# Optimization experiments

Hardware: AMD Instinct MI355X
Metric: run time of the kernel (lower is better)

The kernel has to match this reference:

```python
import jax, jax.numpy as jnp
import numpy as np

C_IN = 256   # c_m
C_H = 32     # outer_product_dim
C_Z = 128
B, S, N = 1, 128, 256  # batch, msa depth, n_res
EPS = 1e-5


def setup_inputs() -> dict:
    key = jax.random.key(0)
    ks = jax.random.split(key, 10)
    msa = jax.random.normal(ks[0], (B, S, N, C_IN), dtype=jnp.float32)
    mask = jax.random.uniform(ks[1], (B, S, N), dtype=jnp.float32)
    ln_w = jnp.ones((C_IN,), jnp.float32)
    ln_b = jnp.zeros((C_IN,), jnp.float32)
    # weights stored [in, out] (torch Linear transposed)
    wl = jax.random.normal(ks[2], (C_IN, C_H), jnp.float32) / np.sqrt(C_IN)
    bl = jnp.zeros((C_H,), jnp.float32)
    wr = jax.random.normal(ks[3], (C_IN, C_H), jnp.float32) / np.sqrt(C_IN)
    br = jnp.zeros((C_H,), jnp.float32)
    wo = jax.random.normal(ks[4], (C_H * C_H, C_Z), jnp.float32) / np.sqrt(C_H * C_H)
    bo = jnp.zeros((C_Z,), jnp.float32)
    return {"msa_representation": msa, "msa_mask": mask, "ln_w": ln_w, "ln_b": ln_b,
            "wl": wl, "bl": bl, "wr": wr, "br": br, "wo": wo, "bo": bo}


def _layer_norm(x, w, b):
    mu = jnp.mean(x, axis=-1, keepdims=True)
    var = jnp.var(x, axis=-1, keepdims=True)
    return (x - mu) * jax.lax.rsqrt(var + EPS) * w + b


def reference(msa_representation, msa_mask, ln_w, ln_b, wl, bl, wr, br, wo, bo):
    x = _layer_norm(msa_representation, ln_w, ln_b)            # [b,s,i,c_in]
    A = x @ wl + bl                                            # [b,s,i,c]
    Bm = x @ wr + br                                           # [b,s,j,d]
    m = msa_mask
    A = A * m[..., None]
    Bm = Bm * m[..., None]
    outer = jnp.einsum('bsic,bsjd->bijcd', A, Bm)              # [b,i,j,c,d]
    norm = jnp.clip(jnp.einsum('bsi,bsj->bij', m, m), 1.0, None)
    mean_val = outer / norm[..., None, None]
    b_, i_, j_ = mean_val.shape[:3]
    mean_val = mean_val.reshape(b_, i_, j_, -1)                # [b,i,j,c*d]
    return mean_val @ wo + bo                                  # [b,i,j,c_z]
```

## Files before the change

kernel.cpp:

```cpp
#include <hip/hip_runtime.h>
#include <hip/hip_bf16.h>
#include <stdint.h>

#define SDEP 128
#define NRES 256
#define CZQ 128

typedef __bf16 v8bf __attribute__((ext_vector_type(8)));
typedef __bf16 v4bf __attribute__((ext_vector_type(4)));
typedef float v16f __attribute__((ext_vector_type(16)));

__device__ __forceinline__ float dpp_wave_sum(float x) {
  float t;
#define STEP(ctrl)                                                         \
  t = __builtin_bit_cast(float, __builtin_amdgcn_update_dpp(               \
          0, __builtin_bit_cast(int, x), ctrl, 0xF, 0xF, true));           \
  x += t;
  STEP(0x111)
  STEP(0x112)
  STEP(0x114)
  STEP(0x118)
  STEP(0x142)
  STEP(0x143)
#undef STEP
  return x;
}
__device__ __forceinline__ float lane63(float x) {
  return __builtin_bit_cast(float,
      __builtin_amdgcn_readlane(__builtin_bit_cast(int, x), 63));
}

#define MFMA32(a, b, c) __builtin_amdgcn_mfma_f32_32x32x16_bf16(a, b, c, 0, 0, 0)

__global__ __launch_bounds__(512, 2) void fusedA_kernel(
    const float* __restrict__ msa, const float* __restrict__ lnw,
    const float* __restrict__ lnb, const float* __restrict__ wl,
    const float* __restrict__ wr, const float* __restrict__ mask,
    const float* __restrict__ wo, const float* __restrict__ bl,
    const float* __restrict__ br,
    __bf16* __restrict__ At2, __bf16* __restrict__ Bt2,
    float* __restrict__ rnorm, __bf16* __restrict__ wot4)
{
  __shared__ __bf16 xs[128 * 258];
  __shared__ __bf16 wcs[16384];
  __shared__ __bf16 Ls[8 * 32 * 36];

  const int i = blockIdx.x, t = threadIdx.x;
  const int w = t >> 6, lane = t & 63;
  const int half = lane >> 5, l31 = lane & 31;
  const int sb = w >> 1, nh = w & 1;

  #pragma unroll
  for (int u = 0; u < 32; ++u) {
    int idx = u * 512 + t;
    int j = idx & 7, n = (idx >> 3) & 31, hf = (idx >> 8) & 1;
    int ks = (idx >> 9) & 15, tile = idx >> 13;
    const float* wsrc = tile ? wr : wl;
    wcs[idx] = (__bf16)wsrc[(ks * 16 + hf * 8 + j) * 32 + n];
  }

  const float4 wv4 = ((const float4*)lnw)[lane];
  const float4 bv4 = ((const float4*)lnb)[lane];

  #pragma unroll 8
  for (int r = 0; r < 16; ++r) {
    const int s = sb * 32 + nh * 16 + r;
    float4 x = ((const float4*)(msa + ((size_t)s * 256 + i) * 256))[lane];
    float s1 = dpp_wave_sum(x.x + x.y + x.z + x.w);
    float s2 = dpp_wave_sum(x.x * x.x + x.y * x.y + x.z * x.z + x.w * x.w);
    float mu = lane63(s1) * (1.f / 256.f);
    float var = lane63(s2) * (1.f / 256.f) - mu * mu;
    float rs = rsqrtf(var + 1e-5f);
    v4bf o;
    o[0] = (__bf16)((x.x - mu) * rs * wv4.x + bv4.x);
    o[1] = (__bf16)((x.y - mu) * rs * wv4.y + bv4.y);
    o[2] = (__bf16)((x.z - mu) * rs * wv4.z + bv4.z);
    o[3] = (__bf16)((x.w - mu) * rs * wv4.w + bv4.w);
    *(v4bf*)(xs + s * 258 + lane * 4) = o;
  }
  __syncthreads();

  v16f acc;
  #pragma unroll
  for (int r = 0; r < 16; ++r) acc[r] = 0.f;

  const __bf16* xrow = xs + (sb * 32 + l31) * 258 + half * 8;
  const __bf16* bbase = wcs + nh * 8192 + half * 256 + l31 * 8;
  #pragma unroll
  for (int ks = 0; ks < 16; ++ks) {
    v8bf a = *(const v8bf*)(xrow + ks * 16);
    v8bf b = *(const v8bf*)(bbase + ks * 512);
    acc = MFMA32(a, b, acc);
  }

  __bf16* Lw = Ls + w * 32 * 36;
  const float bias = (nh ? br : bl)[l31];
  #pragma unroll
  for (int r = 0; r < 16; ++r) {
    int sl = (r & 3) + 8 * (r >> 2) + 4 * half;
    float mv = mask[(sb * 32 + sl) * NRES + i];
    Lw[l31 * 36 + sl] = (__bf16)((acc[r] + bias) * mv);
  }

  __bf16* dst = nh ? Bt2 : At2;
  const int c = lane >> 1, jq = (lane & 1) * 4;
  #pragma unroll
  for (int o = 0; o < 4; ++o) {
    v4bf v = *(const v4bf*)(Lw + c * 36 + o * 8 + jq);
    *(v4bf*)(dst + ((size_t)i * 16 + sb * 4 + o) * 256 + lane * 4) = v;
  }

  if (i < 128) {
    const int b = i * 2 + (t >> 8), col = t & 255;
    float a0 = 0.f;
    #pragma unroll 4
    for (int s = 0; s < SDEP; ++s)
      a0 += mask[s * NRES + b] * mask[s * NRES + col];
    rnorm[b * NRES + col] = 1.f / fmaxf(a0, 1.f);
  } else {
    #pragma unroll
    for (int u = 0; u < 2; ++u) {
      int idx = (i - 128) * 1024 + u * 512 + t;
      int j = idx & 7, lc = (idx >> 3) & 63, kk = (idx >> 9) & 63, zg = idx >> 15;
      int k = kk * 16 + (lc >> 5) * 8 + j;
      int z = zg * 32 + (lc & 31);
      wot4[idx] = (__bf16)wo[k * CZQ + z];
    }
  }
}

__global__ __launch_bounds__(512, 2) void outer_kernel(
    const __bf16* __restrict__ At2, const __bf16* __restrict__ Bt2,
    const float* __restrict__ rnorm, const __bf16* __restrict__ wot4,
    const float* __restrict__ bo, float* __restrict__ out)
{
  __shared__ __bf16 Ps[2][32 * 1032];
  __shared__ __bf16 redb[2][4 * 1024];

  const int tid = threadIdx.x;
  const int w = tid >> 6, lane = tid & 63;
  const int half = lane >> 5, l31 = lane & 31;
  const int bxp = blockIdx.x;
  const int by = blockIdx.y;
  const int mh = w >> 2;
  const int nq = w & 3;
  const int zg = w & 3;
  const int kh = w >> 2;

  const __bf16* Ap  = At2 + ((size_t)(by * 4 + mh * 2)) * 4096 + l31 * 8;
  const __bf16* Bpa = Bt2 + ((size_t)(bxp * 16 + nq * 2)) * 4096 + l31 * 8;
  const __bf16* Bpb = Bpa + 8 * 4096;

  v16f aca[2][2], acb[2][2];
  #pragma unroll
  for (int a = 0; a < 2; ++a)
    #pragma unroll
    for (int b = 0; b < 2; ++b)
      #pragma unroll
      for (int r = 0; r < 16; ++r) { aca[a][b][r] = 0.f; acb[a][b][r] = 0.f; }

  #pragma unroll
  for (int ks = 0; ks < 8; ++ks) {
    const int off = (ks * 2 + half) * 256;
    v8bf a0  = *(const v8bf*)(Ap + off);
    v8bf a1  = *(const v8bf*)(Ap + 4096 + off);
    v8bf b0a = *(const v8bf*)(Bpa + off);
    v8bf b1a = *(const v8bf*)(Bpa + 4096 + off);
    v8bf b0b = *(const v8bf*)(Bpb + off);
    v8bf b1b = *(const v8bf*)(Bpb + 4096 + off);
    aca[0][0] = MFMA32(a0, b0a, aca[0][0]);
    aca[0][1] = MFMA32(a0, b1a, aca[0][1]);
    aca[1][0] = MFMA32(a1, b0a, aca[1][0]);
    aca[1][1] = MFMA32(a1, b1a, aca[1][1]);
    acb[0][0] = MFMA32(a0, b0b, acb[0][0]);
    acb[0][1] = MFMA32(a0, b1b, acb[0][1]);
    acb[1][0] = MFMA32(a1, b0b, acb[1][0]);
    acb[1][1] = MFMA32(a1, b1b, acb[1][1]);
  }

  #pragma unroll
  for (int ti = 0; ti < 2; ++ti) {
    #pragma unroll
    for (int tj = 0; tj < 2; ++tj) {
      const int it = mh * 2 + ti, jt = nq * 2 + tj;
      const int p = it * 8 + jt;
      const float rna = rnorm[(by * 4 + it) * NRES + bxp * 16 + jt];
      const float rnb = rnorm[(by * 4 + it) * NRES + bxp * 16 + 8 + jt];
      #pragma unroll
      for (int r = 0; r < 16; ++r) {
        int cc = (r & 3) + 8 * (r >> 2) + 4 * half;
        Ps[0][p * 1032 + cc * 32 + l31] = (__bf16)(aca[ti][tj][r] * rna);
        Ps[1][p * 1032 + cc * 32 + l31] = (__bf16)(acb[ti][tj][r] * rnb);
      }
    }
  }

  const __bf16* wp =
      wot4 + ((size_t)((zg * 64 + kh * 32) * 64) + half * 32 + l31) * 8;
  v8bf wb[8];
  #pragma unroll
  for (int u = 0; u < 8; ++u)
    wb[u] = *(const v8bf*)(wp + u * 512);
  const float bz = bo[zg * 32 + l31];

  __syncthreads();

  const __bf16* ppa = &Ps[0][l31 * 1032 + kh * 512 + half * 8];
  const __bf16* ppb = &Ps[1][l31 * 1032 + kh * 512 + half * 8];

  v16f c2a, c2b;
  #pragma unroll
  for (int r = 0; r < 16; ++r) { c2a[r] = 0.f; c2b[r] = 0.f; }

  #pragma unroll
  for (int g = 0; g < 4; ++g) {
    #pragma unroll
    for (int u = 0; u < 8; ++u) {
      const int kk = g * 8 + u;
      v8bf bb = wb[u];
      if (g < 3) wb[u] = *(const v8bf*)(wp + (kk + 8) * 512);
      v8bf aaa = *(const v8bf*)(ppa + kk * 16);
      v8bf aab = *(const v8bf*)(ppb + kk * 16);
      c2a = MFMA32(aaa, bb, c2a);
      c2b = MFMA32(aab, bb, c2b);
    }
  }

  if (kh == 1) {
    #pragma unroll
    for (int r = 0; r < 16; ++r) {
      int cc = (r & 3) + 8 * (r >> 2) + 4 * half;
      redb[0][zg * 1024 + cc * 32 + l31] = (__bf16)c2a[r];
      redb[1][zg * 1024 + cc * 32 + l31] = (__bf16)c2b[r];
    }
  }
  __syncthreads();

  if (kh == 0) {
    #pragma unroll
    for (int r = 0; r < 16; ++r) {
      int cc = (r & 3) + 8 * (r >> 2) + 4 * half;
      int i = by * 4 + (cc >> 3);
      float va = c2a[r] + (float)redb[0][zg * 1024 + cc * 32 + l31] + bz;
      float vb = c2b[r] + (float)redb[1][zg * 1024 + cc * 32 + l31] + bz;
      out[((size_t)i * NRES + bxp * 16 + (cc & 7)) * CZQ + zg * 32 + l31] = va;
      out[((size_t)i * NRES + bxp * 16 + 8 + (cc & 7)) * CZQ + zg * 32 + l31] = vb;
    }
  }
}

extern "C" void kernel_launch(void* const* d_in, const int* in_sizes, int n_in,
                              void* d_out, int out_size, void* d_ws, size_t ws_size,
                              hipStream_t stream) {
  const float* msa  = (const float*)d_in[0];
  const float* mask = (const float*)d_in[1];
  const float* lnw  = (const float*)d_in[2];
  const float* lnb  = (const float*)d_in[3];
  const float* wl   = (const float*)d_in[4];
  const float* bl   = (const float*)d_in[5];
  const float* wr   = (const float*)d_in[6];
  const float* br   = (const float*)d_in[7];
  const float* wo   = (const float*)d_in[8];
  const float* bo   = (const float*)d_in[9];
  float* out = (float*)d_out;

  char* ws = (char*)d_ws;
  __bf16* At2   = (__bf16*)(ws);
  __bf16* Bt2   = (__bf16*)(ws + 2097152);
  float*  rnorm = (float*)(ws + 4194304);
  __bf16* wot4  = (__bf16*)(ws + 4456448);

  fusedA_kernel<<<256, 512, 0, stream>>>(msa, lnw, lnb, wl, wr, mask, wo,
                                         bl, br, At2, Bt2, rnorm, wot4);
  outer_kernel<<<dim3(16, 64), 512, 0, stream>>>(At2, Bt2, rnorm, wot4, bo, out);
}
```

Measured before the change: 151.6 us.

## Split fusedA into 1024 smaller blocks with K-split MFMA and register-held weights

The first kernel's grid goes from 256 blocks of 512 threads to 1024 blocks of 256 threads, each block handling one residue and one 32-row MSA slice. The K dimension of the projection GEMM is split across wave pairs and the partial sums are reduced through shared memory. Weight fragments are loaded straight into registers instead of being staged into a 32KB shared tile. The aim is more parallelism and occupancy and less shared memory per block, at the cost of more redundant global weight reads per block and an extra barrier for the reduction.

```diff
diff --git a/kernel.cpp b/kernel.cpp
--- a/kernel.cpp
+++ b/kernel.cpp
@@ -32,7 +32,7 @@
 
 #define MFMA32(a, b, c) __builtin_amdgcn_mfma_f32_32x32x16_bf16(a, b, c, 0, 0, 0)
 
-__global__ __launch_bounds__(512, 2) void fusedA_kernel(
+__global__ __launch_bounds__(256, 4) void fusedA_kernel(
     const float* __restrict__ msa, const float* __restrict__ lnw,
     const float* __restrict__ lnb, const float* __restrict__ wl,
     const float* __restrict__ wr, const float* __restrict__ mask,
@@ -41,30 +41,25 @@
     __bf16* __restrict__ At2, __bf16* __restrict__ Bt2,
     float* __restrict__ rnorm, __bf16* __restrict__ wot4)
 {
-  __shared__ __bf16 xs[128 * 258];
-  __shared__ __bf16 wcs[16384];
-  __shared__ __bf16 Ls[8 * 32 * 36];
-
-  const int i = blockIdx.x, t = threadIdx.x;
+  __shared__ __bf16 xs[32 * 258];
+  __shared__ float  LsF[2 * 1024];
+  __shared__ __bf16 LsT[2 * 32 * 36];
+
+  const int bi = blockIdx.x;
+  const int i = bi >> 2;
+  const int sb = bi & 3;
+  const int t = threadIdx.x;
   const int w = t >> 6, lane = t & 63;
   const int half = lane >> 5, l31 = lane & 31;
-  const int sb = w >> 1, nh = w & 1;
-
-  #pragma unroll
-  for (int u = 0; u < 32; ++u) {
-    int idx = u * 512 + t;
-    int j = idx & 7, n = (idx >> 3) & 31, hf = (idx >> 8) & 1;
-    int ks = (idx >> 9) & 15, tile = idx >> 13;
-    const float* wsrc = tile ? wr : wl;
-    wcs[idx] = (__bf16)wsrc[(ks * 16 + hf * 8 + j) * 32 + n];
-  }
+  const int nh = w & 1;
+  const int kh = w >> 1;
 
   const float4 wv4 = ((const float4*)lnw)[lane];
   const float4 bv4 = ((const float4*)lnb)[lane];
-
-  #pragma unroll 8
-  for (int r = 0; r < 16; ++r) {
-    const int s = sb * 32 + nh * 16 + r;
+  const int s0 = sb * 32 + w * 8;
+  #pragma unroll
+  for (int r = 0; r < 8; ++r) {
+    const int s = s0 + r;
     float4 x = ((const float4*)(msa + ((size_t)s * 256 + i) * 256))[lane];
     float s1 = dpp_wave_sum(x.x + x.y + x.z + x.w);
     float s2 = dpp_wave_sum(x.x * x.x + x.y * x.y + x.z * x.z + x.w * x.w);
@@ -76,56 +71,77 @@
     o[1] = (__bf16)((x.y - mu) * rs * wv4.y + bv4.y);
     o[2] = (__bf16)((x.z - mu) * rs * wv4.z + bv4.z);
     o[3] = (__bf16)((x.w - mu) * rs * wv4.w + bv4.w);
-    *(v4bf*)(xs + s * 258 + lane * 4) = o;
-  }
+    *(v4bf*)(xs + (w * 8 + r) * 258 + lane * 4) = o;
+  }
+
+  const float* wsrc = nh ? wr : wl;
+  v8bf bfr[8];
+  #pragma unroll
+  for (int ks = 0; ks < 8; ++ks) {
+    const int ksg = kh * 8 + ks;
+    float tmp[8];
+    #pragma unroll
+    for (int e = 0; e < 8; ++e)
+      tmp[e] = wsrc[(ksg * 16 + half * 8 + e) * 32 + l31];
+    v8bf bb;
+    #pragma unroll
+    for (int e = 0; e < 8; ++e) bb[e] = (__bf16)tmp[e];
+    bfr[ks] = bb;
+  }
+
   __syncthreads();
 
   v16f acc;
   #pragma unroll
   for (int r = 0; r < 16; ++r) acc[r] = 0.f;
-
-  const __bf16* xrow = xs + (sb * 32 + l31) * 258 + half * 8;
-  const __bf16* bbase = wcs + nh * 8192 + half * 256 + l31 * 8;
-  #pragma unroll
-  for (int ks = 0; ks < 16; ++ks) {
-    v8bf a = *(const v8bf*)(xrow + ks * 16);
-    v8bf b = *(const v8bf*)(bbase + ks * 512);
-    acc = MFMA32(a, b, acc);
-  }
-
-  __bf16* Lw = Ls + w * 32 * 36;
-  const float bias = (nh ? br : bl)[l31];
-  #pragma unroll
-  for (int r = 0; r < 16; ++r) {
-    int sl = (r & 3) + 8 * (r >> 2) + 4 * half;
-    float mv = mask[(sb * 32 + sl) * NRES + i];
-    Lw[l31 * 36 + sl] = (__bf16)((acc[r] + bias) * mv);
-  }
-
-  __bf16* dst = nh ? Bt2 : At2;
-  const int c = lane >> 1, jq = (lane & 1) * 4;
-  #pragma unroll
-  for (int o = 0; o < 4; ++o) {
-    v4bf v = *(const v4bf*)(Lw + c * 36 + o * 8 + jq);
-    *(v4bf*)(dst + ((size_t)i * 16 + sb * 4 + o) * 256 + lane * 4) = v;
-  }
-
-  if (i < 128) {
-    const int b = i * 2 + (t >> 8), col = t & 255;
+  const __bf16* xrow = xs + l31 * 258 + half * 8;
+  #pragma unroll
+  for (int ks = 0; ks < 8; ++ks) {
+    v8bf a = *(const v8bf*)(xrow + (kh * 8 + ks) * 16);
+    acc = MFMA32(a, bfr[ks], acc);
+  }
+
+  if (kh == 1) {
+    #pragma unroll
+    for (int r = 0; r < 16; ++r) {
+      int cc = (r & 3) + 8 * (r >> 2) + 4 * half;
+      LsF[nh * 1024 + cc * 32 + l31] = acc[r];
+    }
+  }
+  __syncthreads();
+
+  if (kh == 0) {
+    const float bias = (nh ? br : bl)[l31];
+    __bf16* Lw = LsT + nh * (32 * 36);
+    #pragma unroll
+    for (int r = 0; r < 16; ++r) {
+      int sl = (r & 3) + 8 * (r >> 2) + 4 * half;
+      float mv = mask[(sb * 32 + sl) * NRES + i];
+      float v = acc[r] + LsF[nh * 1024 + sl * 32 + l31] + bias;
+      Lw[l31 * 36 + sl] = (__bf16)(v * mv);
+    }
+    __bf16* dst = nh ? Bt2 : At2;
+    const int c = lane >> 1, jq = (lane & 1) * 4;
+    #pragma unroll
+    for (int o = 0; o < 4; ++o) {
+      v4bf v = *(const v4bf*)(Lw + c * 36 + o * 8 + jq);
+      *(v4bf*)(dst + ((size_t)i * 16 + sb * 4 + o) * 256 + lane * 4) = v;
+    }
+  }
+
+  if (w == 3) {
+    const int col = sb * 64 + lane;
     float a0 = 0.f;
-    #pragma unroll 4
+    #pragma unroll 8
     for (int s = 0; s < SDEP; ++s)
-      a0 += mask[s * NRES + b] * mask[s * NRES + col];
-    rnorm[b * NRES + col] = 1.f / fmaxf(a0, 1.f);
-  } else {
-    #pragma unroll
-    for (int u = 0; u < 2; ++u) {
-      int idx = (i - 128) * 1024 + u * 512 + t;
-      int j = idx & 7, lc = (idx >> 3) & 63, kk = (idx >> 9) & 63, zg = idx >> 15;
-      int k = kk * 16 + (lc >> 5) * 8 + j;
-      int z = zg * 32 + (lc & 31);
-      wot4[idx] = (__bf16)wo[k * CZQ + z];
-    }
+      a0 += mask[s * NRES + i] * mask[s * NRES + col];
+    rnorm[i * NRES + col] = 1.f / fmaxf(a0, 1.f);
+  } else if (w == 1 || w == 2) {
+    const int idx = bi * 128 + (t - 64);
+    int j = idx & 7, lc = (idx >> 3) & 63, kk = (idx >> 9) & 63, zg = idx >> 15;
+    int k = kk * 16 + (lc >> 5) * 8 + j;
+    int z = zg * 32 + (lc & 31);
+    wot4[idx] = (__bf16)wo[k * CZQ + z];
   }
 }
 
@@ -270,7 +286,7 @@
   float*  rnorm = (float*)(ws + 4194304);
   __bf16* wot4  = (__bf16*)(ws + 4456448);
 
-  fusedA_kernel<<<256, 512, 0, stream>>>(msa, lnw, lnb, wl, wr, mask, wo,
-                                         bl, br, At2, Bt2, rnorm, wot4);
+  fusedA_kernel<<<1024, 256, 0, stream>>>(msa, lnw, lnb, wl, wr, mask, wo,
+                                          bl, br, At2, Bt2, rnorm, wot4);
   outer_kernel<<<dim3(16, 64), 512, 0, stream>>>(At2, Bt2, rnorm, wot4, bo, out);
 }
```

Measured after the change: 148.4 us, median of 2. -2.1%, faster.
